# Performance work log

Measured on AMD Instinct MI355X. Metric: run time of the kernel, lower is better.

Reference implementation:

```python
import jax, jax.numpy as jnp
from jax import lax
import numpy as np

LATENT = 64
NUM_LAYERS = 16
HIDDEN = 16
BATCH = 262144
NEG_SLOPE = 0.01


def setup_inputs() -> dict:
    key = jax.random.key(0)
    ks = jax.random.split(key, 9)
    scale = 0.1
    return {
        "x": jax.random.normal(ks[0], (BATCH, LATENT), dtype=jnp.float32),
        "sW1": scale * jax.random.normal(ks[1], (NUM_LAYERS, HIDDEN, LATENT), dtype=jnp.float32),
        "sb1": scale * jax.random.normal(ks[2], (NUM_LAYERS, HIDDEN), dtype=jnp.float32),
        "sW2": scale * jax.random.normal(ks[3], (NUM_LAYERS, LATENT, HIDDEN), dtype=jnp.float32),
        "sb2": scale * jax.random.normal(ks[4], (NUM_LAYERS, LATENT), dtype=jnp.float32),
        "tW1": scale * jax.random.normal(ks[5], (NUM_LAYERS, HIDDEN, LATENT), dtype=jnp.float32),
        "tb1": scale * jax.random.normal(ks[6], (NUM_LAYERS, HIDDEN), dtype=jnp.float32),
        "tW2": scale * jax.random.normal(ks[7], (NUM_LAYERS, LATENT, HIDDEN), dtype=jnp.float32),
        "tb2": scale * jax.random.normal(ks[8], (NUM_LAYERS, LATENT), dtype=jnp.float32),
    }


def _realnvp_forward(x, sW1, sb1, sW2, sb2, tW1, tb1, tW2, tb2):
    L, d = sW1.shape[0], x.shape[-1]
    # b[i] = 1 - i % 2  -> 1 on even indices; even layers use b, odd layers use 1-b
    base = (jnp.arange(d) % 2 == 0).astype(x.dtype)
    layer_even = (jnp.arange(L) % 2 == 0)[:, None]
    masks = jnp.where(layer_even, base[None, :], 1.0 - base[None, :])  # [L, d]

    def step(carry, p):
        z, ld = carry
        W1s, b1s, W2s, b2s, W1t, b1t, W2t, b2t, m = p
        zm = z * m  # [B, d]
        # s-net: Linear -> LeakyReLU(0.01) -> Linear -> Tanh
        hs = jax.nn.leaky_relu(zm @ W1s.T + b1s, NEG_SLOPE)
        scale = jnp.tanh(hs @ W2s.T + b2s)
        # t-net: Linear -> LeakyReLU(0.01) -> Linear
        ht = jax.nn.leaky_relu(zm @ W1t.T + b1t, NEG_SLOPE)
        trans = ht @ W2t.T + b2t
        # MaskedAffineFlow: z' = b*z + (1-b)*(z*exp(s) + t)
        z = zm + (1.0 - m) * (z * jnp.exp(scale) + trans)
        ld = ld + jnp.sum((1.0 - m) * scale, axis=-1)
        return (z, ld), None

    init = (x, jnp.zeros(x.shape[0], dtype=x.dtype))
    (z, ld), _ = lax.scan(step, init, (sW1, sb1, sW2, sb2, tW1, tb1, tW2, tb2, masks))
    return z[..., None], ld


def reference(x, sW1, sb1, sW2, sb2, tW1, tb1, tW2, tb2):
    return _realnvp_forward(x, sW1, sb1, sW2, sb2, tW1, tb1, tW2, tb2)
```

## Files before the change

### kernel.cpp

```cpp
#include <hip/hip_runtime.h>
#include <hip/hip_bf16.h>

#define NL 16
#define HID 16
#define LAT 64
#define BATCHN 262144

typedef __attribute__((ext_vector_type(4))) float f32x4;
typedef __attribute__((ext_vector_type(8))) short b16x8;

__device__ __forceinline__ f32x4 MFMA32(b16x8 a, b16x8 b, f32x4 c) {
  return __builtin_amdgcn_mfma_f32_16x16x32_bf16(a, b, c, 0, 0, 0);
}

__device__ __forceinline__ unsigned pk2(float lo, float hi) {
  unsigned a = __float_as_uint(lo), b = __float_as_uint(hi);
  a = (a + 0x7fffu + ((a >> 16) & 1u)) >> 16;
  b = (b + 0x7fffu + ((b >> 16) & 1u)) & 0xffff0000u;
  return b | a;
}

#if __has_builtin(__builtin_amdgcn_exp2f)
__device__ __forceinline__ float fexp2(float x) { return __builtin_amdgcn_exp2f(x); }
#else
__device__ __forceinline__ float fexp2(float x) { return __expf(0.6931471805599453f * x); }
#endif
#if __has_builtin(__builtin_amdgcn_rcpf)
__device__ __forceinline__ float frcp(float x) { return __builtin_amdgcn_rcpf(x); }
#else
__device__ __forceinline__ float frcp(float x) { return __fdividef(1.f, x); }
#endif

__device__ __forceinline__ short bfs(float f) {
  union { __hip_bfloat16 h; short s; } u; u.h = __float2bfloat16(f); return u.s;
}
__device__ __forceinline__ float leaky(float v) { return fmaxf(v, 0.01f * v); }
#define TWO_LOG2E 2.885390081777927f
#define LOG2E     1.442695040888963f

__global__ void prep_frags(
    const float* __restrict__ sW1, const float* __restrict__ sb1,
    const float* __restrict__ sW2, const float* __restrict__ sb2,
    const float* __restrict__ tW1, const float* __restrict__ tb1,
    const float* __restrict__ tW2, const float* __restrict__ tb2,
    b16x8* __restrict__ A1S, b16x8* __restrict__ A1T,
    b16x8* __restrict__ A2S, b16x8* __restrict__ A2T,
    f32x4* __restrict__ B1S, f32x4* __restrict__ B1T,
    f32x4* __restrict__ C2S, f32x4* __restrict__ C2T)
{
  const int l = blockIdx.x;
  const int lane = threadIdx.x;
  const int c = lane & 15, g = lane >> 4;
  const int PR = l & 1, PW = 1 - PR;
  const int idx = l * 64 + lane;

  b16x8 a;
  const float* w = sW1 + (l * HID + c) * LAT;
#pragma unroll
  for (int u = 0; u < 8; ++u) a[u] = bfs(w[16 * g + 2 * u + PR]);
  A1S[idx] = a;
  w = tW1 + (l * HID + c) * LAT;
#pragma unroll
  for (int u = 0; u < 8; ++u) a[u] = bfs(w[16 * g + 2 * u + PR]);
  A1T[idx] = a;
  B1S[idx] = ((const f32x4*)(sb1 + l * HID))[g];
  B1T[idx] = ((const f32x4*)(tb1 + l * HID))[g];

#pragma unroll
  for (int to = 0; to < 2; ++to) {
    const int m = 8 * (c >> 2) + 4 * to + (c & 3);
    const int d = 2 * m + PW;
    const int i2 = (l * 2 + to) * 64 + lane;
    b16x8 as = {0, 0, 0, 0, 0, 0, 0, 0}, at = {0, 0, 0, 0, 0, 0, 0, 0};
    const float* w2 = sW2 + (l * LAT + d) * HID + 4 * g;
#pragma unroll
    for (int j = 0; j < 4; ++j) as[j] = bfs(w2[j]);
    w2 = tW2 + (l * LAT + d) * HID + 4 * g;
#pragma unroll
    for (int j = 0; j < 4; ++j) at[4 + j] = bfs(w2[j]);
    A2S[i2] = as;
    A2T[i2] = at;
    f32x4 cs, ct;
#pragma unroll
    for (int j = 0; j < 4; ++j) {
      cs[j] = sb2[l * LAT + 16 * g + 8 * to + 2 * j + PW];
      ct[j] = tb2[l * LAT + 16 * g + 8 * to + 2 * j + PW];
    }
    C2S[i2] = cs;
    C2T[i2] = ct;
  }
}

template<int PR>
__device__ __forceinline__ void layer_step(
    b16x8 a1s, b16x8 a1t, b16x8 a2s0, b16x8 a2s1, b16x8 a2t0, b16x8 a2t1,
    f32x4 b1sv, f32x4 b1tv, f32x4 c2s0, f32x4 c2s1, f32x4 c2t0, f32x4 c2t1,
    f32x4 (&zst)[2][2][2], b16x8 (&zbf)[2][2], float (&ldp)[2])
{
  constexpr int PW = 1 - PR;
#pragma unroll
  for (int T = 0; T < 2; ++T) {
    const f32x4 hs = MFMA32(a1s, zbf[T][PR], b1sv);
    const f32x4 ht = MFMA32(a1t, zbf[T][PR], b1tv);
    union { unsigned u[4]; b16x8 v; } hc;
    hc.u[0] = pk2(leaky(hs[0]), leaky(hs[1]));
    hc.u[1] = pk2(leaky(hs[2]), leaky(hs[3]));
    hc.u[2] = pk2(leaky(ht[0]), leaky(ht[1]));
    hc.u[3] = pk2(leaky(ht[2]), leaky(ht[3]));
    const f32x4 ds0 = MFMA32(a2s0, hc.v, c2s0);
    const f32x4 dt0 = MFMA32(a2t0, hc.v, c2t0);
    const f32x4 ds1 = MFMA32(a2s1, hc.v, c2s1);
    const f32x4 dt1 = MFMA32(a2t1, hc.v, c2t1);
    f32x4 z0 = zst[T][PW][0], z1 = zst[T][PW][1];
#pragma unroll
    for (int j = 0; j < 4; ++j) {
      const float w0 = fexp2(TWO_LOG2E * ds0[j]);
      const float s0 = fmaf(-2.f, frcp(w0 + 1.f), 1.f);
      ldp[T] += s0;
      z0[j] = fmaf(z0[j], fexp2(LOG2E * s0), dt0[j]);
      const float w1 = fexp2(TWO_LOG2E * ds1[j]);
      const float s1 = fmaf(-2.f, frcp(w1 + 1.f), 1.f);
      ldp[T] += s1;
      z1[j] = fmaf(z1[j], fexp2(LOG2E * s1), dt1[j]);
    }
    zst[T][PW][0] = z0;
    zst[T][PW][1] = z1;
    union { unsigned u[4]; b16x8 v; } nz;
    nz.u[0] = pk2(z0[0], z0[1]);
    nz.u[1] = pk2(z0[2], z0[3]);
    nz.u[2] = pk2(z1[0], z1[1]);
    nz.u[3] = pk2(z1[2], z1[3]);
    zbf[T][PW] = nz.v;
  }
}

__global__ __launch_bounds__(256) void realnvp_fwd(
    const float* __restrict__ x, float* __restrict__ out,
    const b16x8* __restrict__ A1S, const b16x8* __restrict__ A1T,
    const b16x8* __restrict__ A2S, const b16x8* __restrict__ A2T,
    const f32x4* __restrict__ B1S, const f32x4* __restrict__ B1T,
    const f32x4* __restrict__ C2S, const f32x4* __restrict__ C2T)
{
  const int lane = threadIdx.x & 63;
  const int wv = threadIdx.x >> 6;
  const int c = lane & 15, g = lane >> 4;
  const int rowbase = (blockIdx.x * 4 + wv) * 32;

  f32x4 zst[2][2][2];
  b16x8 zbf[2][2];
  float ldp[2] = {0.f, 0.f};
#pragma unroll
  for (int T = 0; T < 2; ++T) {
    const f32x4* xr = (const f32x4*)(x + (size_t)(rowbase + T * 16 + c) * LAT);
    const f32x4 q0 = xr[4 * g], q1 = xr[4 * g + 1], q2 = xr[4 * g + 2], q3 = xr[4 * g + 3];
    zst[T][0][0] = (f32x4){q0[0], q0[2], q1[0], q1[2]};
    zst[T][1][0] = (f32x4){q0[1], q0[3], q1[1], q1[3]};
    zst[T][0][1] = (f32x4){q2[0], q2[2], q3[0], q3[2]};
    zst[T][1][1] = (f32x4){q2[1], q2[3], q3[1], q3[3]};
#pragma unroll
    for (int p = 0; p < 2; ++p) {
      union { unsigned u[4]; b16x8 v; } zb;
      zb.u[0] = pk2(zst[T][p][0][0], zst[T][p][0][1]);
      zb.u[1] = pk2(zst[T][p][0][2], zst[T][p][0][3]);
      zb.u[2] = pk2(zst[T][p][1][0], zst[T][p][1][1]);
      zb.u[3] = pk2(zst[T][p][1][2], zst[T][p][1][3]);
      zbf[T][p] = zb.v;
    }
  }

#pragma unroll 1
  for (int lp = 0; lp < NL / 2; ++lp) {
    {
      const int i1 = (2 * lp) * 64 + lane, i2 = (4 * lp) * 64 + lane;
      layer_step<0>(A1S[i1], A1T[i1], A2S[i2], A2S[i2 + 64], A2T[i2], A2T[i2 + 64],
                    B1S[i1], B1T[i1], C2S[i2], C2S[i2 + 64], C2T[i2], C2T[i2 + 64],
                    zst, zbf, ldp);
    }
    {
      const int i1 = (2 * lp + 1) * 64 + lane, i2 = (4 * lp + 2) * 64 + lane;
      layer_step<1>(A1S[i1], A1T[i1], A2S[i2], A2S[i2 + 64], A2T[i2], A2T[i2 + 64],
                    B1S[i1], B1T[i1], C2S[i2], C2S[i2 + 64], C2T[i2], C2T[i2 + 64],
                    zst, zbf, ldp);
    }
  }

#pragma unroll
  for (int T = 0; T < 2; ++T) {
    f32x4* zo = (f32x4*)(out + (size_t)(rowbase + T * 16 + c) * LAT);
    const f32x4 e0 = zst[T][0][0], o0 = zst[T][1][0];
    const f32x4 e1 = zst[T][0][1], o1 = zst[T][1][1];
    zo[4 * g]     = (f32x4){e0[0], o0[0], e0[1], o0[1]};
    zo[4 * g + 1] = (f32x4){e0[2], o0[2], e0[3], o0[3]};
    zo[4 * g + 2] = (f32x4){e1[0], o1[0], e1[1], o1[1]};
    zo[4 * g + 3] = (f32x4){e1[2], o1[2], e1[3], o1[3]};
  }
#pragma unroll
  for (int T = 0; T < 2; ++T) {
    ldp[T] += __shfl_xor(ldp[T], 16, 64);
    ldp[T] += __shfl_xor(ldp[T], 32, 64);
  }
  if (g < 2)
    out[(size_t)BATCHN * LAT + rowbase + g * 16 + c] = g ? ldp[1] : ldp[0];
}

extern "C" void kernel_launch(void* const* d_in, const int* in_sizes, int n_in,
                              void* d_out, int out_size, void* d_ws, size_t ws_size,
                              hipStream_t stream) {
  const float* x   = (const float*)d_in[0];
  const float* sW1 = (const float*)d_in[1];
  const float* sb1 = (const float*)d_in[2];
  const float* sW2 = (const float*)d_in[3];
  const float* sb2 = (const float*)d_in[4];
  const float* tW1 = (const float*)d_in[5];
  const float* tb1 = (const float*)d_in[6];
  const float* tW2 = (const float*)d_in[7];
  const float* tb2 = (const float*)d_in[8];
  float* out = (float*)d_out;

  char* w = (char*)d_ws;
  b16x8* A1S = (b16x8*)w;            w += NL * 64 * sizeof(b16x8);
  b16x8* A1T = (b16x8*)w;            w += NL * 64 * sizeof(b16x8);
  b16x8* A2S = (b16x8*)w;            w += NL * 128 * sizeof(b16x8);
  b16x8* A2T = (b16x8*)w;            w += NL * 128 * sizeof(b16x8);
  f32x4* B1S = (f32x4*)w;            w += NL * 64 * sizeof(f32x4);
  f32x4* B1T = (f32x4*)w;            w += NL * 64 * sizeof(f32x4);
  f32x4* C2S = (f32x4*)w;            w += NL * 128 * sizeof(f32x4);
  f32x4* C2T = (f32x4*)w;            w += NL * 128 * sizeof(f32x4);

  hipLaunchKernelGGL(prep_frags, dim3(NL), dim3(64), 0, stream,
                     sW1, sb1, sW2, sb2, tW1, tb1, tW2, tb2,
                     A1S, A1T, A2S, A2T, B1S, B1T, C2S, C2T);
  hipLaunchKernelGGL(realnvp_fwd, dim3(BATCHN / 128), dim3(256), 0, stream,
                     x, out, A1S, A1T, A2S, A2T, B1S, B1T, C2S, C2T);
}
```

Before: 112.4 us.

## Process four row tiles per wave and pack bf16 operands on demand

```diff
diff --git a/kernel.cpp b/kernel.cpp
--- a/kernel.cpp
+++ b/kernel.cpp
@@ -95,13 +95,18 @@
 __device__ __forceinline__ void layer_step(
     b16x8 a1s, b16x8 a1t, b16x8 a2s0, b16x8 a2s1, b16x8 a2t0, b16x8 a2t1,
     f32x4 b1sv, f32x4 b1tv, f32x4 c2s0, f32x4 c2s1, f32x4 c2t0, f32x4 c2t1,
-    f32x4 (&zst)[2][2][2], b16x8 (&zbf)[2][2], float (&ldp)[2])
+    f32x4 (&zst)[4][2][2], float (&ldp)[4])
 {
   constexpr int PW = 1 - PR;
 #pragma unroll
-  for (int T = 0; T < 2; ++T) {
-    const f32x4 hs = MFMA32(a1s, zbf[T][PR], b1sv);
-    const f32x4 ht = MFMA32(a1t, zbf[T][PR], b1tv);
+  for (int T = 0; T < 4; ++T) {
+    union { unsigned u[4]; b16x8 v; } zB;
+    zB.u[0] = pk2(zst[T][PR][0][0], zst[T][PR][0][1]);
+    zB.u[1] = pk2(zst[T][PR][0][2], zst[T][PR][0][3]);
+    zB.u[2] = pk2(zst[T][PR][1][0], zst[T][PR][1][1]);
+    zB.u[3] = pk2(zst[T][PR][1][2], zst[T][PR][1][3]);
+    const f32x4 hs = MFMA32(a1s, zB.v, b1sv);
+    const f32x4 ht = MFMA32(a1t, zB.v, b1tv);
     union { unsigned u[4]; b16x8 v; } hc;
     hc.u[0] = pk2(leaky(hs[0]), leaky(hs[1]));
     hc.u[1] = pk2(leaky(hs[2]), leaky(hs[3]));
@@ -111,26 +116,19 @@
     const f32x4 dt0 = MFMA32(a2t0, hc.v, c2t0);
     const f32x4 ds1 = MFMA32(a2s1, hc.v, c2s1);
     const f32x4 dt1 = MFMA32(a2t1, hc.v, c2t1);
-    f32x4 z0 = zst[T][PW][0], z1 = zst[T][PW][1];
 #pragma unroll
     for (int j = 0; j < 4; ++j) {
       const float w0 = fexp2(TWO_LOG2E * ds0[j]);
-      const float s0 = fmaf(-2.f, frcp(w0 + 1.f), 1.f);
-      ldp[T] += s0;
-      z0[j] = fmaf(z0[j], fexp2(LOG2E * s0), dt0[j]);
+      const float r0 = frcp(w0 + 1.f);
+      ldp[T] += fmaf(-2.f, r0, 1.f);
+      zst[T][PW][0][j] = fmaf(zst[T][PW][0][j],
+                              fexp2(fmaf(-2.f * LOG2E, r0, LOG2E)), dt0[j]);
       const float w1 = fexp2(TWO_LOG2E * ds1[j]);
-      const float s1 = fmaf(-2.f, frcp(w1 + 1.f), 1.f);
-      ldp[T] += s1;
-      z1[j] = fmaf(z1[j], fexp2(LOG2E * s1), dt1[j]);
-    }
-    zst[T][PW][0] = z0;
-    zst[T][PW][1] = z1;
-    union { unsigned u[4]; b16x8 v; } nz;
-    nz.u[0] = pk2(z0[0], z0[1]);
-    nz.u[1] = pk2(z0[2], z0[3]);
-    nz.u[2] = pk2(z1[0], z1[1]);
-    nz.u[3] = pk2(z1[2], z1[3]);
-    zbf[T][PW] = nz.v;
+      const float r1 = frcp(w1 + 1.f);
+      ldp[T] += fmaf(-2.f, r1, 1.f);
+      zst[T][PW][1][j] = fmaf(zst[T][PW][1][j],
+                              fexp2(fmaf(-2.f * LOG2E, r1, LOG2E)), dt1[j]);
+    }
   }
 }
 
@@ -144,28 +142,18 @@
   const int lane = threadIdx.x & 63;
   const int wv = threadIdx.x >> 6;
   const int c = lane & 15, g = lane >> 4;
-  const int rowbase = (blockIdx.x * 4 + wv) * 32;
-
-  f32x4 zst[2][2][2];
-  b16x8 zbf[2][2];
-  float ldp[2] = {0.f, 0.f};
-#pragma unroll
-  for (int T = 0; T < 2; ++T) {
+  const int rowbase = (blockIdx.x * 4 + wv) * 64;
+
+  f32x4 zst[4][2][2];
+  float ldp[4] = {0.f, 0.f, 0.f, 0.f};
+#pragma unroll
+  for (int T = 0; T < 4; ++T) {
     const f32x4* xr = (const f32x4*)(x + (size_t)(rowbase + T * 16 + c) * LAT);
     const f32x4 q0 = xr[4 * g], q1 = xr[4 * g + 1], q2 = xr[4 * g + 2], q3 = xr[4 * g + 3];
     zst[T][0][0] = (f32x4){q0[0], q0[2], q1[0], q1[2]};
     zst[T][1][0] = (f32x4){q0[1], q0[3], q1[1], q1[3]};
     zst[T][0][1] = (f32x4){q2[0], q2[2], q3[0], q3[2]};
     zst[T][1][1] = (f32x4){q2[1], q2[3], q3[1], q3[3]};
-#pragma unroll
-    for (int p = 0; p < 2; ++p) {
-      union { unsigned u[4]; b16x8 v; } zb;
-      zb.u[0] = pk2(zst[T][p][0][0], zst[T][p][0][1]);
-      zb.u[1] = pk2(zst[T][p][0][2], zst[T][p][0][3]);
-      zb.u[2] = pk2(zst[T][p][1][0], zst[T][p][1][1]);
-      zb.u[3] = pk2(zst[T][p][1][2], zst[T][p][1][3]);
-      zbf[T][p] = zb.v;
-    }
   }
 
 #pragma unroll 1
@@ -174,18 +162,18 @@
       const int i1 = (2 * lp) * 64 + lane, i2 = (4 * lp) * 64 + lane;
       layer_step<0>(A1S[i1], A1T[i1], A2S[i2], A2S[i2 + 64], A2T[i2], A2T[i2 + 64],
                     B1S[i1], B1T[i1], C2S[i2], C2S[i2 + 64], C2T[i2], C2T[i2 + 64],
-                    zst, zbf, ldp);
+                    zst, ldp);
     }
     {
       const int i1 = (2 * lp + 1) * 64 + lane, i2 = (4 * lp + 2) * 64 + lane;
       layer_step<1>(A1S[i1], A1T[i1], A2S[i2], A2S[i2 + 64], A2T[i2], A2T[i2 + 64],
                     B1S[i1], B1T[i1], C2S[i2], C2S[i2 + 64], C2T[i2], C2T[i2 + 64],
-                    zst, zbf, ldp);
-    }
-  }
-
-#pragma unroll
-  for (int T = 0; T < 2; ++T) {
+                    zst, ldp);
+    }
+  }
+
+#pragma unroll
+  for (int T = 0; T < 4; ++T) {
     f32x4* zo = (f32x4*)(out + (size_t)(rowbase + T * 16 + c) * LAT);
     const f32x4 e0 = zst[T][0][0], o0 = zst[T][1][0];
     const f32x4 e1 = zst[T][0][1], o1 = zst[T][1][1];
@@ -195,12 +183,13 @@
     zo[4 * g + 3] = (f32x4){e1[2], o1[2], e1[3], o1[3]};
   }
 #pragma unroll
-  for (int T = 0; T < 2; ++T) {
+  for (int T = 0; T < 4; ++T) {
     ldp[T] += __shfl_xor(ldp[T], 16, 64);
     ldp[T] += __shfl_xor(ldp[T], 32, 64);
   }
-  if (g < 2)
-    out[(size_t)BATCHN * LAT + rowbase + g * 16 + c] = g ? ldp[1] : ldp[0];
+  const float lo = (g & 1) ? ldp[1] : ldp[0];
+  const float hi = (g & 1) ? ldp[3] : ldp[2];
+  out[(size_t)BATCHN * LAT + rowbase + g * 16 + c] = (g & 2) ? hi : lo;
 }
 
 extern "C" void kernel_launch(void* const* d_in, const int* in_sizes, int n_in,
@@ -230,6 +219,6 @@
   hipLaunchKernelGGL(prep_frags, dim3(NL), dim3(64), 0, stream,
                      sW1, sb1, sW2, sb2, tW1, tb1, tW2, tb2,
                      A1S, A1T, A2S, A2T, B1S, B1T, C2S, C2T);
-  hipLaunchKernelGGL(realnvp_fwd, dim3(BATCHN / 128), dim3(256), 0, stream,
+  hipLaunchKernelGGL(realnvp_fwd, dim3(BATCHN / 256), dim3(256), 0, stream,
                      x, out, A1S, A1T, A2S, A2T, B1S, B1T, C2S, C2T);
 }
```

After: 121.1 us. +7.7%, slower.
